# Kernel optimization log

Measured on AMD Instinct MI355X. Metric: run time of the kernel, lower is better.

Reference implementation:

```python
import jax, jax.numpy as jnp
import numpy as np

D = 512; H = 8; L = 6; DFF = 2048; V = 32000
B = 2; S_SRC = 1024; S_TRG = 1024
PAD_ID = 0
DH = D // H

def posenc(S, d):
    pos = np.arange(S)[:, None].astype(np.float32)
    i = np.arange(0, d, 2)[None, :].astype(np.float32)
    ang = pos / (10000.0 ** (i / d))
    pe = np.zeros((S, d), np.float32)
    pe[:, 0::2] = np.sin(ang)
    pe[:, 1::2] = np.cos(ang)
    return jnp.asarray(pe)

def layernorm(x, s, b):
    m = jnp.mean(x, -1, keepdims=True)
    v = jnp.var(x, -1, keepdims=True)
    return (x - m) * jax.lax.rsqrt(v + 1e-5) * s + b

def split_heads(x):
    b, s, _ = x.shape
    return x.reshape(b, s, H, DH).transpose(0, 2, 1, 3)  # [B,H,S,DH]

def merge_heads(x):
    b, h, s, dh = x.shape
    return x.transpose(0, 2, 1, 3).reshape(b, s, h * dh)

def attn(q, k, v, mask):
    # q,k,v: [B,H,Sq,DH]/[B,H,Sk,DH]; mask True = blocked, broadcastable to [B,H,Sq,Sk]
    scores = jnp.einsum('bhqd,bhkd->bhqk', q, k) * (DH ** -0.5)
    scores = jnp.where(mask, -1e9, scores)
    p = jax.nn.softmax(scores, axis=-1)
    return merge_heads(jnp.einsum('bhqk,bhkd->bhqd', p, v))

def setup_inputs() -> dict:
    key = jax.random.key(0)
    ks = iter(jax.random.split(key, 64))
    g = lambda shape, s=0.02: (jax.random.normal(next(ks), shape, jnp.float32) * s)
    inp = {}
    inp['batch_src'] = jax.random.randint(next(ks), (B, S_SRC), 0, V, jnp.int32)
    inp['trg_teacher'] = jax.random.randint(next(ks), (B, S_TRG), 0, V, jnp.int32)
    inp['src_emb'] = g((V, D)); inp['trg_emb'] = g((V, D))
    inp['fc_w'] = g((D, V)); inp['fc_b'] = jnp.zeros((V,), jnp.float32)
    # encoder layer stacks [L, ...]
    inp['enc_wqkv'] = g((L, D, 3 * D)); inp['enc_wo'] = g((L, D, D))
    inp['enc_ln1s'] = jnp.ones((L, D)); inp['enc_ln1b'] = jnp.zeros((L, D))
    inp['enc_w1'] = g((L, D, DFF)); inp['enc_b1'] = jnp.zeros((L, DFF))
    inp['enc_w2'] = g((L, DFF, D)); inp['enc_b2'] = jnp.zeros((L, D))
    inp['enc_ln2s'] = jnp.ones((L, D)); inp['enc_ln2b'] = jnp.zeros((L, D))
    # decoder layer stacks
    inp['dec_wqkv'] = g((L, D, 3 * D)); inp['dec_wo'] = g((L, D, D))
    inp['dec_ln1s'] = jnp.ones((L, D)); inp['dec_ln1b'] = jnp.zeros((L, D))
    inp['dec_wq'] = g((L, D, D)); inp['dec_wkv'] = g((L, D, 2 * D))
    inp['dec_woc'] = g((L, D, D))
    inp['dec_ln2s'] = jnp.ones((L, D)); inp['dec_ln2b'] = jnp.zeros((L, D))
    inp['dec_w1'] = g((L, D, DFF)); inp['dec_b1'] = jnp.zeros((L, DFF))
    inp['dec_w2'] = g((L, DFF, D)); inp['dec_b2'] = jnp.zeros((L, D))
    inp['dec_ln3s'] = jnp.ones((L, D)); inp['dec_ln3b'] = jnp.zeros((L, D))
    return inp

def reference(batch_src, trg_teacher, src_emb, trg_emb, fc_w, fc_b,
              enc_wqkv, enc_wo, enc_ln1s, enc_ln1b, enc_w1, enc_b1, enc_w2, enc_b2, enc_ln2s, enc_ln2b,
              dec_wqkv, dec_wo, dec_ln1s, dec_ln1b, dec_wq, dec_wkv, dec_woc, dec_ln2s, dec_ln2b,
              dec_w1, dec_b1, dec_w2, dec_b2, dec_ln3s, dec_ln3b):
    enc_mask = (batch_src == PAD_ID)[:, None, None, :]             # [B,1,1,S_src]
    causal = jnp.triu(jnp.ones((S_TRG, S_TRG), bool), 1)[None, None]  # [1,1,S,S]

    # ---- encoder ----
    x = src_emb[batch_src] * (D ** 0.5) + posenc(S_SRC, D)

    def enc_layer(x, p):
        wqkv, wo, l1s, l1b, w1, b1, w2, b2, l2s, l2b = p
        q, k, v = jnp.split(x @ wqkv, 3, axis=-1)
        o = attn(split_heads(q), split_heads(k), split_heads(v), enc_mask) @ wo
        x = layernorm(x + o, l1s, l1b)
        h = jax.nn.relu(x @ w1 + b1) @ w2 + b2
        return layernorm(x + h, l2s, l2b), None

    enc_out, _ = jax.lax.scan(enc_layer, x,
        (enc_wqkv, enc_wo, enc_ln1s, enc_ln1b, enc_w1, enc_b1, enc_w2, enc_b2, enc_ln2s, enc_ln2b))

    # ---- decoder (teacher forcing) ----
    y = trg_emb[trg_teacher] * (D ** 0.5) + posenc(S_TRG, D)

    def dec_layer(y, p):
        (wqkv, wo, l1s, l1b, wq, wkv, woc, l2s, l2b, w1, b1, w2, b2, l3s, l3b) = p
        q, k, v = jnp.split(y @ wqkv, 3, axis=-1)
        o = attn(split_heads(q), split_heads(k), split_heads(v), causal) @ wo
        y = layernorm(y + o, l1s, l1b)
        qc = y @ wq
        kc, vc = jnp.split(enc_out @ wkv, 2, axis=-1)
        oc = attn(split_heads(qc), split_heads(kc), split_heads(vc), enc_mask) @ woc
        y = layernorm(y + oc, l2s, l2b)
        h = jax.nn.relu(y @ w1 + b1) @ w2 + b2
        return layernorm(y + h, l3s, l3b), None

    dec_out, _ = jax.lax.scan(dec_layer, y,
        (dec_wqkv, dec_wo, dec_ln1s, dec_ln1b, dec_wq, dec_wkv, dec_woc, dec_ln2s, dec_ln2b,
         dec_w1, dec_b1, dec_w2, dec_b2, dec_ln3s, dec_ln3b))

    logits = dec_out @ fc_w + fc_b  # [B, S_TRG, V]
    return logits
```

## Files before the change

kernel.cpp:

```cpp
#include <hip/hip_runtime.h>
#include <cmath>

#define Dm   512
#define Hn   8
#define Ln   6
#define DFFm 2048
#define Vm   32000
#define Bn   2
#define Sn   1024
#define DHm  64
#define Mrows (Bn*Sn)

typedef unsigned short ushort_t;
typedef __attribute__((ext_vector_type(8))) short          s16x8;
typedef __attribute__((ext_vector_type(8))) unsigned short u16x8;
typedef __attribute__((ext_vector_type(4))) float          f32x4;

__device__ __forceinline__ ushort_t f2bf(float x) {
    union { float f; unsigned u; } un; un.f = x;
    unsigned r = un.u + 0x7fffu + ((un.u >> 16) & 1u);
    return (ushort_t)(r >> 16);
}

template<int TR, int NW>
__device__ __forceinline__ void stage_tile(const ushort_t* __restrict__ src, int ld,
                                           ushort_t* lds, int k0, int w, int lane)
{
    constexpr int CH = TR / (8 * NW);
    #pragma unroll
    for (int c = 0; c < CH; ++c) {
        const int rb = (w * CH + c) * 8;
        const int r  = rb + (lane >> 3);
        const ushort_t* gp = src + (size_t)r * ld + k0
                           + (((lane & 7) ^ ((lane >> 3) & 7)) << 3);
        __builtin_amdgcn_global_load_lds(
            (const __attribute__((address_space(1))) void*)gp,
            (__attribute__((address_space(3))) void*)(lds + rb * 64),
            16, 0, 0);
    }
}

__device__ __forceinline__ s16x8 ldrd(const ushort_t* lds, int r, int st)
{
    return *(const s16x8*)&lds[r * 64 + ((st ^ (r & 7)) << 3)];
}

template<int TM, int TN, int NW, bool OBF, bool BIAS, bool RELU, bool VTOUT, bool SWZ, bool RES>
__global__ __launch_bounds__(NW * 64) void gemm_bf(
    const ushort_t* __restrict__ A, const ushort_t* __restrict__ Bt,
    void* __restrict__ Cv, const float* __restrict__ bias,
    int K, int lda, int ldb, int ldc,
    long A_sb, long A_sh, long B_sb, long B_sh, long C_sb, long C_sh, int nh,
    ushort_t* __restrict__ VTp, int voff, const float* __restrict__ Xres)
{
    constexpr int WC = NW / 2;
    constexpr int FI = TM / 32;
    constexpr int FJ = TN / (16 * WC);
    __shared__ __align__(16) ushort_t As[2][TM * 64];
    __shared__ __align__(16) ushort_t Bs[2][TN * 64];

    const int z = blockIdx.z, b = z / nh, h = z - b * nh;
    A  += (size_t)b * A_sb + (size_t)h * A_sh;
    Bt += (size_t)b * B_sb + (size_t)h * B_sh;

    int bx = blockIdx.x, by = blockIdx.y;
    if constexpr (SWZ) {
        const int ncol = gridDim.x, nrow = gridDim.y;
        const int total = ncol * nrow;
        const int flat = bx + by * ncol;
        const int per = total >> 3;
        const int g = (flat & 7) * per + (flat >> 3);
        bx = g / nrow;
        by = g - bx * nrow;
    }

    const int tid  = threadIdx.x;
    const int w    = tid >> 6, lane = tid & 63;
    const int m0   = by * TM, n0 = bx * TN;
    const int rw   = (w / WC) * (TM / 2);
    const int cn   = (w % WC) * (TN / WC);
    const int l15  = lane & 15, l4 = lane >> 4;

    const ushort_t* Ab = A + (size_t)m0 * lda;
    const ushort_t* Bb = Bt + (size_t)n0 * ldb;

    f32x4 acc[FI][FJ] = {};

    stage_tile<TM, NW>(Ab, lda, As[0], 0, w, lane);
    stage_tile<TN, NW>(Bb, ldb, Bs[0], 0, w, lane);
    __syncthreads();

    const int nk = K >> 6;
    for (int t = 0; t < nk; ++t) {
        const int cur = t & 1;
        if (t + 1 < nk) {
            stage_tile<TM, NW>(Ab, lda, As[cur ^ 1], (t + 1) << 6, w, lane);
            stage_tile<TN, NW>(Bb, ldb, Bs[cur ^ 1], (t + 1) << 6, w, lane);
        }
        #pragma unroll
        for (int ks = 0; ks < 2; ++ks) {
            const int st = ks * 4 + l4;
            s16x8 av[FI], bv[FJ];
            #pragma unroll
            for (int i = 0; i < FI; ++i) av[i] = ldrd(As[cur], rw + i * 16 + l15, st);
            #pragma unroll
            for (int j = 0; j < FJ; ++j) bv[j] = ldrd(Bs[cur], cn + j * 16 + l15, st);
            #pragma unroll
            for (int i = 0; i < FI; ++i)
                #pragma unroll
                for (int j = 0; j < FJ; ++j)
                    acc[i][j] = __builtin_amdgcn_mfma_f32_16x16x32_bf16(
                                    av[i], bv[j], acc[i][j], 0, 0, 0);
        }
        __syncthreads();
    }

    const int colb = n0 + cn + l15;
    const int rowb = m0 + rw + (l4 << 2);
    float bvv[FJ];
    #pragma unroll
    for (int j = 0; j < FJ; ++j) bvv[j] = BIAS ? bias[colb + j * 16] : 0.f;

    if constexpr (OBF) {
        ushort_t* C = (ushort_t*)Cv + (size_t)b * C_sb + (size_t)h * C_sh;
        #pragma unroll
        for (int i = 0; i < FI; ++i)
            #pragma unroll
            for (int r = 0; r < 4; ++r) {
                const int row = rowb + i * 16 + r;
                #pragma unroll
                for (int j = 0; j < FJ; ++j) {
                    float v = acc[i][j][r] + bvv[j];
                    if (RELU) v = fmaxf(v, 0.f);
                    const int col = colb + j * 16;
                    if (VTOUT && col >= voff) {
                        const int hc = (col - voff) >> 6, d = (col - voff) & 63;
                        const int zz = (row >> 10) * 8 + hc;
                        VTp[(size_t)zz * (64 * Sn) + (size_t)d * Sn + (row & (Sn - 1))] = f2bf(v);
                    } else {
                        C[(size_t)row * ldc + col] = f2bf(v);
                    }
                }
            }
    } else {
        float* C = (float*)Cv + (size_t)b * C_sb + (size_t)h * C_sh;
        #pragma unroll
        for (int i = 0; i < FI; ++i)
            #pragma unroll
            for (int r = 0; r < 4; ++r) {
                const size_t row = rowb + i * 16 + r;
                #pragma unroll
                for (int j = 0; j < FJ; ++j) {
                    float v = acc[i][j][r] + bvv[j];
                    if (RES) v += Xres[row * ldc + colb + j * 16];
                    if (RELU) v = fmaxf(v, 0.f);
                    C[row * ldc + colb + j * 16] = v;
                }
            }
    }
}

template<int MODE>
__global__ __launch_bounds__(512) void flash_attn(
    const ushort_t* __restrict__ Qp, const ushort_t* __restrict__ Kp,
    const ushort_t* __restrict__ VTp, ushort_t* __restrict__ AO,
    const int* __restrict__ tok, int ldq, int ldk)
{
    __shared__ __align__(16) ushort_t Ks[2][2][64 * 64];
    __shared__ __align__(16) ushort_t Vs[2][2][64 * 64];
    __shared__ __align__(16) ushort_t Ps[8][16 * 64];
    __shared__ float msk[Sn];
    __shared__ float mrg[4][64][25];

    const int z = blockIdx.y, b = z >> 3, h = z & 7;
    const int qb = blockIdx.x * 64;
    const int tid = threadIdx.x, w = tid >> 6, lane = tid & 63;
    const int g = w >> 2, w4 = w & 3;
    const int l15 = lane & 15, l4 = lane >> 4;

    const ushort_t* Qbase = Qp + (size_t)b * Sn * ldq + h * 64;
    const ushort_t* Kbase = Kp + (size_t)b * Sn * ldk + h * 64;
    const ushort_t* Vbase = VTp + (size_t)z * 64 * Sn;
    ushort_t* Obase = AO + ((size_t)(b * Sn + qb)) * Dm + h * 64;

    if (MODE == 0) {
        const int* tb = tok + (size_t)b * Sn;
        for (int i = tid; i < Sn; i += 512) msk[i] = (tb[i] == 0) ? 1.f : 0.f;
    }

    const int qrow = qb + w4 * 16 + l15;
    s16x8 qv[2];
    qv[0] = *(const s16x8*)(Qbase + (size_t)qrow * ldq + l4 * 8);
    qv[1] = *(const s16x8*)(Qbase + (size_t)qrow * ldq + 32 + l4 * 8);

    f32x4 o[4] = {};
    float m[4], lsum[4];
    #pragma unroll
    for (int r = 0; r < 4; ++r) { m[r] = -1e30f; lsum[r] = 0.f; }

    const int nt = (MODE == 1) ? (qb / 64 + 1) : (Sn / 64);
    const int nIt = (nt + 1) >> 1;

    if (g < nt) {
        stage_tile<64, 4>(Kbase + (size_t)(g * 64) * ldk, ldk, Ks[g][0], 0, w4, lane);
        stage_tile<64, 4>(Vbase, Sn, Vs[g][0], g * 64, w4, lane);
    }
    __syncthreads();

    for (int it = 0; it < nIt; ++it) {
        const int kt = 2 * it + g;
        const int cur = it & 1;
        if (kt + 2 < nt) {
            stage_tile<64, 4>(Kbase + (size_t)((kt + 2) * 64) * ldk, ldk, Ks[g][cur ^ 1], 0, w4, lane);
            stage_tile<64, 4>(Vbase, Sn, Vs[g][cur ^ 1], (kt + 2) * 64, w4, lane);
        }
        if (kt < nt) {
            f32x4 s[4] = {};
            #pragma unroll
            for (int ks = 0; ks < 2; ++ks) {
                const int st = ks * 4 + l4;
                #pragma unroll
                for (int j = 0; j < 4; ++j) {
                    s16x8 bv = ldrd(Ks[g][cur], j * 16 + l15, st);
                    s[j] = __builtin_amdgcn_mfma_f32_16x16x32_bf16(qv[ks], bv, s[j], 0, 0, 0);
                }
            }

            #pragma unroll
            for (int j = 0; j < 4; ++j) {
                const int col = kt * 64 + j * 16 + l15;
                #pragma unroll
                for (int r = 0; r < 4; ++r) {
                    float v = s[j][r] * 0.125f;
                    if (MODE == 0) { if (msk[col] != 0.f) v = -1e9f; }
                    else           { if (col > qb + w4 * 16 + l4 * 4 + r) v = -1e9f; }
                    s[j][r] = v;
                }
            }

            float mt[4];
            #pragma unroll
            for (int r = 0; r < 4; ++r)
                mt[r] = fmaxf(fmaxf(s[0][r], s[1][r]), fmaxf(s[2][r], s[3][r]));
            #pragma unroll
            for (int mk = 1; mk < 16; mk <<= 1)
                #pragma unroll
                for (int r = 0; r < 4; ++r)
                    mt[r] = fmaxf(mt[r], __shfl_xor(mt[r], mk));

            float al[4];
            #pragma unroll
            for (int r = 0; r < 4; ++r) {
                const float mn = fmaxf(m[r], mt[r]);
                al[r] = __expf(m[r] - mn);
                m[r] = mn;
            }

            float rs[4] = {0.f, 0.f, 0.f, 0.f};
            ushort_t* pw = Ps[w];
            #pragma unroll
            for (int j = 0; j < 4; ++j) {
                const int slot = j * 2 + (l15 >> 3), e = l15 & 7;
                #pragma unroll
                for (int r = 0; r < 4; ++r) {
                    const float pvv = __expf(s[j][r] - m[r]);
                    rs[r] += pvv;
                    const int row = l4 * 4 + r;
                    pw[row * 64 + ((slot ^ (row & 7)) << 3) + e] = f2bf(pvv);
                }
            }
            #pragma unroll
            for (int mk = 1; mk < 16; mk <<= 1)
                #pragma unroll
                for (int r = 0; r < 4; ++r)
                    rs[r] += __shfl_xor(rs[r], mk);
            #pragma unroll
            for (int r = 0; r < 4; ++r) lsum[r] = lsum[r] * al[r] + rs[r];

            #pragma unroll
            for (int jd = 0; jd < 4; ++jd)
                #pragma unroll
                for (int r = 0; r < 4; ++r)
                    o[jd][r] *= al[r];
            #pragma unroll
            for (int ks2 = 0; ks2 < 2; ++ks2) {
                const int st2 = ks2 * 4 + l4;
                s16x8 pa = ldrd(pw, l15, st2);
                #pragma unroll
                for (int jd = 0; jd < 4; ++jd) {
                    s16x8 bv2 = ldrd(Vs[g][cur], jd * 16 + l15, st2);
                    o[jd] = __builtin_amdgcn_mfma_f32_16x16x32_bf16(pa, bv2, o[jd], 0, 0, 0);
                }
            }
        }
        __syncthreads();
    }

    if (g == 1) {
        float* mp = mrg[w4][lane];
        #pragma unroll
        for (int jd = 0; jd < 4; ++jd)
            #pragma unroll
            for (int r = 0; r < 4; ++r)
                mp[jd * 4 + r] = o[jd][r];
        #pragma unroll
        for (int r = 0; r < 4; ++r) { mp[16 + r] = m[r]; mp[20 + r] = lsum[r]; }
    }
    __syncthreads();
    if (g == 0) {
        const float* mp = mrg[w4][lane];
        float a0[4], a1[4], inv[4];
        #pragma unroll
        for (int r = 0; r < 4; ++r) {
            const float m1 = mp[16 + r];
            const float mm = fmaxf(m[r], m1);
            a0[r] = __expf(m[r] - mm);
            a1[r] = __expf(m1 - mm);
            inv[r] = 1.f / (lsum[r] * a0[r] + mp[20 + r] * a1[r]);
        }
        #pragma unroll
        for (int jd = 0; jd < 4; ++jd)
            #pragma unroll
            for (int r = 0; r < 4; ++r)
                Obase[(size_t)(w4 * 16 + l4 * 4 + r) * Dm + jd * 16 + l15] =
                    f2bf((o[jd][r] * a0[r] + mp[jd * 4 + r] * a1[r]) * inv[r]);
    }
}

struct WEnt { const float* src; ushort_t* dst; int R, C, tile0; };
struct WPack { WEnt e[12]; };

__global__ __launch_bounds__(256) void wcvt_all(WPack p)
{
    const int bid = blockIdx.x;
    int i = 0;
    #pragma unroll
    for (int k = 1; k < 12; ++k) if (bid >= p.e[k].tile0) i = k;
    const WEnt wd = p.e[i];
    const int rel = bid - wd.tile0;
    const int tC = wd.C >> 5, tR = wd.R >> 5;
    const int tpl = tC * tR;
    const int l = rel / tpl, t2 = rel - l * tpl;
    const int ty = t2 / tC, tx = t2 - ty * tC;

    const float* in  = wd.src + (size_t)l * wd.R * wd.C;
    ushort_t*    out = wd.dst + (size_t)l * wd.R * wd.C;

    __shared__ float tbuf[32][33];
    const int r0 = ty * 32, c0 = tx * 32;
    const int tid = threadIdx.x;
    const int r = tid >> 5, c = tid & 31;
    #pragma unroll
    for (int q = 0; q < 4; ++q)
        tbuf[r + q * 8][c] = in[(size_t)(r0 + r + q * 8) * wd.C + c0 + c];
    __syncthreads();
    const int c2 = tid >> 5, r2 = tid & 31;
    #pragma unroll
    for (int q = 0; q < 4; ++q)
        out[(size_t)(c0 + c2 + q * 8) * wd.R + r0 + r2] = f2bf(tbuf[r2][c2 + q * 8]);
}

__global__ __launch_bounds__(256) void ln_only(
    const float* __restrict__ s_in, float* __restrict__ x,
    const float* __restrict__ s, const float* __restrict__ bb,
    ushort_t* __restrict__ xbf)
{
    const long row = blockIdx.x;
    const int t = threadIdx.x;
    const float* sr = s_in + row * Dm;
    float v0 = sr[t];
    float v1 = sr[t + 256];

    float sum = v0 + v1, ssq = v0 * v0 + v1 * v1;
    __shared__ float red[8];
    for (int off = 32; off; off >>= 1) {
        sum += __shfl_down(sum, off);
        ssq += __shfl_down(ssq, off);
    }
    const int lane = t & 63, w = t >> 6;
    if (lane == 0) { red[w] = sum; red[4 + w] = ssq; }
    __syncthreads();
    sum = red[0] + red[1] + red[2] + red[3];
    ssq = red[4] + red[5] + red[6] + red[7];

    const float mean = sum * (1.f / Dm);
    const float var  = ssq * (1.f / Dm) - mean * mean;
    const float r = rsqrtf(var + 1e-5f);
    const float r0 = (v0 - mean) * r * s[t] + bb[t];
    const float r1 = (v1 - mean) * r * s[t + 256] + bb[t + 256];
    x[row * Dm + t] = r0; x[row * Dm + t + 256] = r1;
    xbf[row * Dm + t] = f2bf(r0);
    xbf[row * Dm + t + 256] = f2bf(r1);
}

__global__ __launch_bounds__(256) void embed_pe(
    const int* __restrict__ tokA, const float* __restrict__ embA,
    float* __restrict__ outA, ushort_t* __restrict__ outbfA,
    const int* __restrict__ tokB, const float* __restrict__ embB,
    float* __restrict__ outB, ushort_t* __restrict__ outbfB)
{
    const int bs = blockIdx.x;
    const int s = bs % Sn;
    const int t = threadIdx.x;
    const int*      tok   = blockIdx.y ? tokB : tokA;
    const float*    emb   = blockIdx.y ? embB : embA;
    float*          out   = blockIdx.y ? outB : outA;
    ushort_t*       outbf = blockIdx.y ? outbfB : outbfA;
    const int token = tok[bs];
    #pragma unroll
    for (int r = 0; r < 2; ++r) {
        const int d = t + r * 256;
        const int i = d & ~1;
        const float ang = (float)s * powf(10000.0f, -(float)i / (float)Dm);
        const float pe = (d & 1) ? cosf(ang) : sinf(ang);
        const float v = emb[(size_t)token * Dm + d] * 22.627416997969522f + pe;
        out[(size_t)bs * Dm + d] = v;
        outbf[(size_t)bs * Dm + d] = f2bf(v);
    }
}

extern "C" void kernel_launch(void* const* d_in, const int* in_sizes, int n_in,
                              void* d_out, int out_size, void* d_ws, size_t ws_size,
                              hipStream_t stream)
{
    const int*   batch_src = (const int*)d_in[0];
    const int*   trg       = (const int*)d_in[1];
    const float* src_emb   = (const float*)d_in[2];
    const float* trg_emb   = (const float*)d_in[3];
    const float* fc_w      = (const float*)d_in[4];
    const float* fc_b      = (const float*)d_in[5];
    const float* enc_wqkv  = (const float*)d_in[6];
    const float* enc_wo    = (const float*)d_in[7];
    const float* enc_ln1s  = (const float*)d_in[8];
    const float* enc_ln1b  = (const float*)d_in[9];
    const float* enc_w1    = (const float*)d_in[10];
    const float* enc_b1    = (const float*)d_in[11];
    const float* enc_w2    = (const float*)d_in[12];
    const float* enc_b2    = (const float*)d_in[13];
    const float* enc_ln2s  = (const float*)d_in[14];
    const float* enc_ln2b  = (const float*)d_in[15];
    const float* dec_wqkv  = (const float*)d_in[16];
    const float* dec_wo    = (const float*)d_in[17];
    const float* dec_ln1s  = (const float*)d_in[18];
    const float* dec_ln1b  = (const float*)d_in[19];
    const float* dec_wq    = (const float*)d_in[20];
    const float* dec_wkv   = (const float*)d_in[21];
    const float* dec_woc   = (const float*)d_in[22];
    const float* dec_ln2s  = (const float*)d_in[23];
    const float* dec_ln2b  = (const float*)d_in[24];
    const float* dec_w1    = (const float*)d_in[25];
    const float* dec_b1    = (const float*)d_in[26];
    const float* dec_w2    = (const float*)d_in[27];
    const float* dec_b2    = (const float*)d_in[28];
    const float* dec_ln3s  = (const float*)d_in[29];
    const float* dec_ln3b  = (const float*)d_in[30];
    (void)in_sizes; (void)n_in; (void)out_size; (void)ws_size;

    char* p = (char*)d_ws;
    auto alloc = [&](size_t bytes) { char* r = p; p += (bytes + 255) & ~(size_t)255; return r; };
    float*    X     = (float*)alloc((size_t)Mrows * Dm * 4);
    float*    Y     = (float*)alloc((size_t)Mrows * Dm * 4);
    float*    O     = (float*)alloc((size_t)Mrows * Dm * 4);
    ushort_t* Xbf   = (ushort_t*)alloc((size_t)Mrows * Dm * 2);
    ushort_t* Ybf   = (ushort_t*)alloc((size_t)Mrows * Dm * 2);
    ushort_t* QKVbf = (ushort_t*)alloc((size_t)Mrows * 3 * Dm * 2);
    ushort_t* AObf  = (ushort_t*)alloc((size_t)Mrows * Dm * 2);
    ushort_t* FHbf  = (ushort_t*)alloc((size_t)Mrows * DFFm * 2);
    ushort_t* QCbf  = (ushort_t*)alloc((size_t)Mrows * Dm * 2);
    ushort_t* KVbf  = (ushort_t*)alloc((size_t)Mrows * 2 * Dm * 2);
    ushort_t* VT    = (ushort_t*)alloc((size_t)16 * DHm * Sn * 2);
    ushort_t* ewqkv_t = (ushort_t*)alloc((size_t)Ln * 3 * Dm * Dm * 2);
    ushort_t* ewo_t   = (ushort_t*)alloc((size_t)Ln * Dm * Dm * 2);
    ushort_t* ew1_t   = (ushort_t*)alloc((size_t)Ln * DFFm * Dm * 2);
    ushort_t* ew2_t   = (ushort_t*)alloc((size_t)Ln * Dm * DFFm * 2);
    ushort_t* dwqkv_t = (ushort_t*)alloc((size_t)Ln * 3 * Dm * Dm * 2);
    ushort_t* dwo_t   = (ushort_t*)alloc((size_t)Ln * Dm * Dm * 2);
    ushort_t* dwq_t   = (ushort_t*)alloc((size_t)Ln * Dm * Dm * 2);
    ushort_t* dwkv_t  = (ushort_t*)alloc((size_t)Ln * 2 * Dm * Dm * 2);
    ushort_t* dwoc_t  = (ushort_t*)alloc((size_t)Ln * Dm * Dm * 2);
    ushort_t* dw1_t   = (ushort_t*)alloc((size_t)Ln * DFFm * Dm * 2);
    ushort_t* dw2_t   = (ushort_t*)alloc((size_t)Ln * Dm * DFFm * 2);
    ushort_t* fcw_t   = (ushort_t*)alloc((size_t)Vm * Dm * 2);

    {
        WPack pk;
        auto set = [&](int i, const float* s, ushort_t* d, int R, int C, int nl, int& acc) {
            pk.e[i] = { s, d, R, C, acc };
            acc += (R >> 5) * (C >> 5) * nl;
        };
        int acc = 0;
        set(0,  enc_wqkv, ewqkv_t, Dm,   3 * Dm, Ln, acc);
        set(1,  enc_wo,   ewo_t,   Dm,   Dm,     Ln, acc);
        set(2,  enc_w1,   ew1_t,   Dm,   DFFm,   Ln, acc);
        set(3,  enc_w2,   ew2_t,   DFFm, Dm,     Ln, acc);
        set(4,  dec_wqkv, dwqkv_t, Dm,   3 * Dm, Ln, acc);
        set(5,  dec_wo,   dwo_t,   Dm,   Dm,     Ln, acc);
        set(6,  dec_wq,   dwq_t,   Dm,   Dm,     Ln, acc);
        set(7,  dec_wkv,  dwkv_t,  Dm,   2 * Dm, Ln, acc);
        set(8,  dec_woc,  dwoc_t,  Dm,   Dm,     Ln, acc);
        set(9,  dec_w1,   dw1_t,   Dm,   DFFm,   Ln, acc);
        set(10, dec_w2,   dw2_t,   DFFm, Dm,     Ln, acc);
        set(11, fc_w,     fcw_t,   Dm,   Vm,     1,  acc);
        wcvt_all<<<acc, 256, 0, stream>>>(pk);
    }

    embed_pe<<<dim3(Mrows, 2), 256, 0, stream>>>(
        batch_src, src_emb, X, Xbf, trg, trg_emb, Y, Ybf);

    for (int l = 0; l < Ln; ++l) {
        gemm_bf<64,128,8,true,false,false,true,false,false><<<dim3(12, 32, 1), 512, 0, stream>>>(
            Xbf, ewqkv_t + (size_t)l * 3 * Dm * Dm, QKVbf, nullptr,
            Dm, Dm, Dm, 3 * Dm, 0,0,0,0,0,0, 1, VT, 2 * Dm, nullptr);
        flash_attn<0><<<dim3(16, 16), 512, 0, stream>>>(
            QKVbf, QKVbf + Dm, VT, AObf, batch_src, 3 * Dm, 3 * Dm);
        gemm_bf<64,64,8,false,false,false,false,false,true><<<dim3(8, 32, 1), 512, 0, stream>>>(
            AObf, ewo_t + (size_t)l * Dm * Dm, O, nullptr,
            Dm, Dm, Dm, Dm, 0,0,0,0,0,0, 1, nullptr, 0, X);
        ln_only<<<Mrows, 256, 0, stream>>>(O, X, enc_ln1s + l * Dm, enc_ln1b + l * Dm, Xbf);
        gemm_bf<64,128,8,true,true,true,false,false,false><<<dim3(16, 32, 1), 512, 0, stream>>>(
            Xbf, ew1_t + (size_t)l * DFFm * Dm, FHbf, enc_b1 + l * DFFm,
            Dm, Dm, Dm, DFFm, 0,0,0,0,0,0, 1, nullptr, 0, nullptr);
        gemm_bf<64,64,8,false,true,false,false,false,true><<<dim3(8, 32, 1), 512, 0, stream>>>(
            FHbf, ew2_t + (size_t)l * Dm * DFFm, O, enc_b2 + l * Dm,
            DFFm, DFFm, DFFm, Dm, 0,0,0,0,0,0, 1, nullptr, 0, X);
        ln_only<<<Mrows, 256, 0, stream>>>(O, X, enc_ln2s + l * Dm, enc_ln2b + l * Dm, Xbf);
    }

    for (int l = 0; l < Ln; ++l) {
        gemm_bf<64,128,8,true,false,false,true,false,false><<<dim3(12, 32, 1), 512, 0, stream>>>(
            Ybf, dwqkv_t + (size_t)l * 3 * Dm * Dm, QKVbf, nullptr,
            Dm, Dm, Dm, 3 * Dm, 0,0,0,0,0,0, 1, VT, 2 * Dm, nullptr);
        flash_attn<1><<<dim3(16, 16), 512, 0, stream>>>(
            QKVbf, QKVbf + Dm, VT, AObf, nullptr, 3 * Dm, 3 * Dm);
        gemm_bf<64,64,8,false,false,false,false,false,true><<<dim3(8, 32, 1), 512, 0, stream>>>(
            AObf, dwo_t + (size_t)l * Dm * Dm, O, nullptr,
            Dm, Dm, Dm, Dm, 0,0,0,0,0,0, 1, nullptr, 0, Y);
        ln_only<<<Mrows, 256, 0, stream>>>(O, Y, dec_ln1s + l * Dm, dec_ln1b + l * Dm, Ybf);

        gemm_bf<64,64,8,true,false,false,false,false,false><<<dim3(8, 32, 1), 512, 0, stream>>>(
            Ybf, dwq_t + (size_t)l * Dm * Dm, QCbf, nullptr,
            Dm, Dm, Dm, Dm, 0,0,0,0,0,0, 1, nullptr, 0, nullptr);
        gemm_bf<64,128,8,true,false,false,true,false,false><<<dim3(8, 32, 1), 512, 0, stream>>>(
            Xbf, dwkv_t + (size_t)l * 2 * Dm * Dm, KVbf, nullptr,
            Dm, Dm, Dm, 2 * Dm, 0,0,0,0,0,0, 1, VT, Dm, nullptr);
        flash_attn<0><<<dim3(16, 16), 512, 0, stream>>>(
            QCbf, KVbf, VT, AObf, batch_src, Dm, 2 * Dm);
        gemm_bf<64,64,8,false,false,false,false,false,true><<<dim3(8, 32, 1), 512, 0, stream>>>(
            AObf, dwoc_t + (size_t)l * Dm * Dm, O, nullptr,
            Dm, Dm, Dm, Dm, 0,0,0,0,0,0, 1, nullptr, 0, Y);
        ln_only<<<Mrows, 256, 0, stream>>>(O, Y, dec_ln2s + l * Dm, dec_ln2b + l * Dm, Ybf);

        gemm_bf<64,128,8,true,true,true,false,false,false><<<dim3(16, 32, 1), 512, 0, stream>>>(
            Ybf, dw1_t + (size_t)l * DFFm * Dm, FHbf, dec_b1 + l * DFFm,
            Dm, Dm, Dm, DFFm, 0,0,0,0,0,0, 1, nullptr, 0, nullptr);
        gemm_bf<64,64,8,false,true,false,false,false,true><<<dim3(8, 32, 1), 512, 0, stream>>>(
            FHbf, dw2_t + (size_t)l * Dm * DFFm, O, dec_b2 + l * Dm,
            DFFm, DFFm, DFFm, Dm, 0,0,0,0,0,0, 1, nullptr, 0, Y);
        ln_only<<<Mrows, 256, 0, stream>>>(O, Y, dec_ln3s + l * Dm, dec_ln3b + l * Dm, Ybf);
    }

    gemm_bf<128,128,8,false,true,false,false,true,false><<<dim3(Vm / 128, 16, 1), 512, 0, stream>>>(
        Ybf, fcw_t, (float*)d_out, fc_b,
        Dm, Dm, Dm, Vm, 0,0,0,0,0,0, 1, nullptr, 0, nullptr);
}
```

Before: 1.593 ms.

## Batch cross-attention KV projections for all layers and fuse decoder Q projections

Cross-attention K/V projections of the encoder output run once for all six decoder layers in a single batched GEMM (grid z = layers), writing into per-layer KV and V-transpose caches. The decoder's self-attention QKV weights and cross-attention Q weights are packed into one 4*D-wide matrix, so one GEMM replaces two per layer. Several GEMM instantiations also drop from 8 to 4 waves per block. This cuts launches and gives larger grids, at the cost of extra workspace and changed per-thread tiling.

```diff
diff --git a/kernel.cpp b/kernel.cpp
--- a/kernel.cpp
+++ b/kernel.cpp
@@ -51,7 +51,7 @@
     void* __restrict__ Cv, const float* __restrict__ bias,
     int K, int lda, int ldb, int ldc,
     long A_sb, long A_sh, long B_sb, long B_sh, long C_sb, long C_sh, int nh,
-    ushort_t* __restrict__ VTp, int voff, const float* __restrict__ Xres)
+    ushort_t* __restrict__ VTp, int voff, long VT_sz, const float* __restrict__ Xres)
 {
     constexpr int WC = NW / 2;
     constexpr int FI = TM / 32;
@@ -62,6 +62,7 @@
     const int z = blockIdx.z, b = z / nh, h = z - b * nh;
     A  += (size_t)b * A_sb + (size_t)h * A_sh;
     Bt += (size_t)b * B_sb + (size_t)h * B_sh;
+    ushort_t* VTl = VTp + (size_t)z * VT_sz;
 
     int bx = blockIdx.x, by = blockIdx.y;
     if constexpr (SWZ) {
@@ -133,10 +134,10 @@
                     float v = acc[i][j][r] + bvv[j];
                     if (RELU) v = fmaxf(v, 0.f);
                     const int col = colb + j * 16;
-                    if (VTOUT && col >= voff) {
+                    if (VTOUT && col >= voff && col < voff + 512) {
                         const int hc = (col - voff) >> 6, d = (col - voff) & 63;
                         const int zz = (row >> 10) * 8 + hc;
-                        VTp[(size_t)zz * (64 * Sn) + (size_t)d * Sn + (row & (Sn - 1))] = f2bf(v);
+                        VTl[(size_t)zz * (64 * Sn) + (size_t)d * Sn + (row & (Sn - 1))] = f2bf(v);
                     } else {
                         C[(size_t)row * ldc + col] = f2bf(v);
                     }
@@ -327,7 +328,7 @@
     }
 }
 
-struct WEnt { const float* src; ushort_t* dst; int R, C, tile0; };
+struct WEnt { const float* src; ushort_t* dst; int R, C, tile0; long dls; };
 struct WPack { WEnt e[12]; };
 
 __global__ __launch_bounds__(256) void wcvt_all(WPack p)
@@ -344,7 +345,7 @@
     const int ty = t2 / tC, tx = t2 - ty * tC;
 
     const float* in  = wd.src + (size_t)l * wd.R * wd.C;
-    ushort_t*    out = wd.dst + (size_t)l * wd.R * wd.C;
+    ushort_t*    out = wd.dst + (size_t)l * wd.dls;
 
     __shared__ float tbuf[32][33];
     const int r0 = ty * 32, c0 = tx * 32;
@@ -464,18 +465,18 @@
     ushort_t* Xbf   = (ushort_t*)alloc((size_t)Mrows * Dm * 2);
     ushort_t* Ybf   = (ushort_t*)alloc((size_t)Mrows * Dm * 2);
     ushort_t* QKVbf = (ushort_t*)alloc((size_t)Mrows * 3 * Dm * 2);
+    ushort_t* QKVQ  = (ushort_t*)alloc((size_t)Mrows * 4 * Dm * 2);
     ushort_t* AObf  = (ushort_t*)alloc((size_t)Mrows * Dm * 2);
     ushort_t* FHbf  = (ushort_t*)alloc((size_t)Mrows * DFFm * 2);
-    ushort_t* QCbf  = (ushort_t*)alloc((size_t)Mrows * Dm * 2);
-    ushort_t* KVbf  = (ushort_t*)alloc((size_t)Mrows * 2 * Dm * 2);
     ushort_t* VT    = (ushort_t*)alloc((size_t)16 * DHm * Sn * 2);
+    ushort_t* KVC   = (ushort_t*)alloc((size_t)Ln * Mrows * 2 * Dm * 2);
+    ushort_t* VTC   = (ushort_t*)alloc((size_t)Ln * 16 * DHm * Sn * 2);
     ushort_t* ewqkv_t = (ushort_t*)alloc((size_t)Ln * 3 * Dm * Dm * 2);
     ushort_t* ewo_t   = (ushort_t*)alloc((size_t)Ln * Dm * Dm * 2);
     ushort_t* ew1_t   = (ushort_t*)alloc((size_t)Ln * DFFm * Dm * 2);
     ushort_t* ew2_t   = (ushort_t*)alloc((size_t)Ln * Dm * DFFm * 2);
-    ushort_t* dwqkv_t = (ushort_t*)alloc((size_t)Ln * 3 * Dm * Dm * 2);
+    ushort_t* dwqkvq_t= (ushort_t*)alloc((size_t)Ln * 4 * Dm * Dm * 2);
     ushort_t* dwo_t   = (ushort_t*)alloc((size_t)Ln * Dm * Dm * 2);
-    ushort_t* dwq_t   = (ushort_t*)alloc((size_t)Ln * Dm * Dm * 2);
     ushort_t* dwkv_t  = (ushort_t*)alloc((size_t)Ln * 2 * Dm * Dm * 2);
     ushort_t* dwoc_t  = (ushort_t*)alloc((size_t)Ln * Dm * Dm * 2);
     ushort_t* dw1_t   = (ushort_t*)alloc((size_t)Ln * DFFm * Dm * 2);
@@ -484,82 +485,87 @@
 
     {
         WPack pk;
-        auto set = [&](int i, const float* s, ushort_t* d, int R, int C, int nl, int& acc) {
-            pk.e[i] = { s, d, R, C, acc };
+        auto set = [&](int i, const float* s, ushort_t* d, int R, int C, int nl,
+                       long dls, int& acc) {
+            pk.e[i] = { s, d, R, C, acc, dls };
             acc += (R >> 5) * (C >> 5) * nl;
         };
         int acc = 0;
-        set(0,  enc_wqkv, ewqkv_t, Dm,   3 * Dm, Ln, acc);
-        set(1,  enc_wo,   ewo_t,   Dm,   Dm,     Ln, acc);
-        set(2,  enc_w1,   ew1_t,   Dm,   DFFm,   Ln, acc);
-        set(3,  enc_w2,   ew2_t,   DFFm, Dm,     Ln, acc);
-        set(4,  dec_wqkv, dwqkv_t, Dm,   3 * Dm, Ln, acc);
-        set(5,  dec_wo,   dwo_t,   Dm,   Dm,     Ln, acc);
-        set(6,  dec_wq,   dwq_t,   Dm,   Dm,     Ln, acc);
-        set(7,  dec_wkv,  dwkv_t,  Dm,   2 * Dm, Ln, acc);
-        set(8,  dec_woc,  dwoc_t,  Dm,   Dm,     Ln, acc);
-        set(9,  dec_w1,   dw1_t,   Dm,   DFFm,   Ln, acc);
-        set(10, dec_w2,   dw2_t,   DFFm, Dm,     Ln, acc);
-        set(11, fc_w,     fcw_t,   Dm,   Vm,     1,  acc);
+        const long L4 = (long)4 * Dm * Dm;
+        set(0,  enc_wqkv, ewqkv_t, Dm,   3 * Dm, Ln, (long)3 * Dm * Dm, acc);
+        set(1,  enc_wo,   ewo_t,   Dm,   Dm,     Ln, (long)Dm * Dm,     acc);
+        set(2,  enc_w1,   ew1_t,   Dm,   DFFm,   Ln, (long)Dm * DFFm,   acc);
+        set(3,  enc_w2,   ew2_t,   DFFm, Dm,     Ln, (long)Dm * DFFm,   acc);
+        set(4,  dec_wqkv, dwqkvq_t,                Dm, 3 * Dm, Ln, L4,  acc);
+        set(5,  dec_wq,   dwqkvq_t + (size_t)3 * Dm * Dm, Dm, Dm, Ln, L4, acc);
+        set(6,  dec_wo,   dwo_t,   Dm,   Dm,     Ln, (long)Dm * Dm,     acc);
+        set(7,  dec_wkv,  dwkv_t,  Dm,   2 * Dm, Ln, (long)2 * Dm * Dm, acc);
+        set(8,  dec_woc,  dwoc_t,  Dm,   Dm,     Ln, (long)Dm * Dm,     acc);
+        set(9,  dec_w1,   dw1_t,   Dm,   DFFm,   Ln, (long)Dm * DFFm,   acc);
+        set(10, dec_w2,   dw2_t,   DFFm, Dm,     Ln, (long)Dm * DFFm,   acc);
+        set(11, fc_w,     fcw_t,   Dm,   Vm,     1,  (long)Dm * Vm,     acc);
         wcvt_all<<<acc, 256, 0, stream>>>(pk);
     }
 
     embed_pe<<<dim3(Mrows, 2), 256, 0, stream>>>(
         batch_src, src_emb, X, Xbf, trg, trg_emb, Y, Ybf);
 
+    const long VTs = (long)16 * DHm * Sn;
+
     for (int l = 0; l < Ln; ++l) {
-        gemm_bf<64,128,8,true,false,false,true,false,false><<<dim3(12, 32, 1), 512, 0, stream>>>(
+        gemm_bf<64,128,4,true,false,false,true,false,false><<<dim3(12, 32, 1), 256, 0, stream>>>(
             Xbf, ewqkv_t + (size_t)l * 3 * Dm * Dm, QKVbf, nullptr,
-            Dm, Dm, Dm, 3 * Dm, 0,0,0,0,0,0, 1, VT, 2 * Dm, nullptr);
+            Dm, Dm, Dm, 3 * Dm, 0,0,0,0,0,0, 1, VT, 2 * Dm, 0, nullptr);
         flash_attn<0><<<dim3(16, 16), 512, 0, stream>>>(
             QKVbf, QKVbf + Dm, VT, AObf, batch_src, 3 * Dm, 3 * Dm);
         gemm_bf<64,64,8,false,false,false,false,false,true><<<dim3(8, 32, 1), 512, 0, stream>>>(
             AObf, ewo_t + (size_t)l * Dm * Dm, O, nullptr,
-            Dm, Dm, Dm, Dm, 0,0,0,0,0,0, 1, nullptr, 0, X);
+            Dm, Dm, Dm, Dm, 0,0,0,0,0,0, 1, nullptr, 0, 0, X);
         ln_only<<<Mrows, 256, 0, stream>>>(O, X, enc_ln1s + l * Dm, enc_ln1b + l * Dm, Xbf);
-        gemm_bf<64,128,8,true,true,true,false,false,false><<<dim3(16, 32, 1), 512, 0, stream>>>(
+        gemm_bf<64,128,4,true,true,true,false,false,false><<<dim3(16, 32, 1), 256, 0, stream>>>(
             Xbf, ew1_t + (size_t)l * DFFm * Dm, FHbf, enc_b1 + l * DFFm,
-            Dm, Dm, Dm, DFFm, 0,0,0,0,0,0, 1, nullptr, 0, nullptr);
+            Dm, Dm, Dm, DFFm, 0,0,0,0,0,0, 1, nullptr, 0, 0, nullptr);
         gemm_bf<64,64,8,false,true,false,false,false,true><<<dim3(8, 32, 1), 512, 0, stream>>>(
             FHbf, ew2_t + (size_t)l * Dm * DFFm, O, enc_b2 + l * Dm,
-            DFFm, DFFm, DFFm, Dm, 0,0,0,0,0,0, 1, nullptr, 0, X);
+            DFFm, DFFm, DFFm, Dm, 0,0,0,0,0,0, 1, nullptr, 0, 0, X);
         ln_only<<<Mrows, 256, 0, stream>>>(O, X, enc_ln2s + l * Dm, enc_ln2b + l * Dm, Xbf);
     }
 
+    gemm_bf<64,128,4,true,false,false,true,false,false><<<dim3(8, 32, Ln), 256, 0, stream>>>(
+        Xbf, dwkv_t, KVC, nullptr,
+        Dm, Dm, Dm, 2 * Dm,
+        0, 0, (long)2 * Dm * Dm, 0, (long)Mrows * 2 * Dm, 0, 1,
+        VTC, Dm, VTs, nullptr);
+
     for (int l = 0; l < Ln; ++l) {
-        gemm_bf<64,128,8,true,false,false,true,false,false><<<dim3(12, 32, 1), 512, 0, stream>>>(
-            Ybf, dwqkv_t + (size_t)l * 3 * Dm * Dm, QKVbf, nullptr,
-            Dm, Dm, Dm, 3 * Dm, 0,0,0,0,0,0, 1, VT, 2 * Dm, nullptr);
+        gemm_bf<64,128,4,true,false,false,true,false,false><<<dim3(16, 32, 1), 256, 0, stream>>>(
+            Ybf, dwqkvq_t + (size_t)l * 4 * Dm * Dm, QKVQ, nullptr,
+            Dm, Dm, Dm, 4 * Dm, 0,0,0,0,0,0, 1, VT, 2 * Dm, 0, nullptr);
         flash_attn<1><<<dim3(16, 16), 512, 0, stream>>>(
-            QKVbf, QKVbf + Dm, VT, AObf, nullptr, 3 * Dm, 3 * Dm);
+            QKVQ, QKVQ + Dm, VT, AObf, nullptr, 4 * Dm, 4 * Dm);
         gemm_bf<64,64,8,false,false,false,false,false,true><<<dim3(8, 32, 1), 512, 0, stream>>>(
             AObf, dwo_t + (size_t)l * Dm * Dm, O, nullptr,
-            Dm, Dm, Dm, Dm, 0,0,0,0,0,0, 1, nullptr, 0, Y);
+            Dm, Dm, Dm, Dm, 0,0,0,0,0,0, 1, nullptr, 0, 0, Y);
         ln_only<<<Mrows, 256, 0, stream>>>(O, Y, dec_ln1s + l * Dm, dec_ln1b + l * Dm, Ybf);
 
-        gemm_bf<64,64,8,true,false,false,false,false,false><<<dim3(8, 32, 1), 512, 0, stream>>>(
-            Ybf, dwq_t + (size_t)l * Dm * Dm, QCbf, nullptr,
-            Dm, Dm, Dm, Dm, 0,0,0,0,0,0, 1, nullptr, 0, nullptr);
-        gemm_bf<64,128,8,true,false,false,true,false,false><<<dim3(8, 32, 1), 512, 0, stream>>>(
-            Xbf, dwkv_t + (size_t)l * 2 * Dm * Dm, KVbf, nullptr,
-            Dm, Dm, Dm, 2 * Dm, 0,0,0,0,0,0, 1, VT, Dm, nullptr);
         flash_attn<0><<<dim3(16, 16), 512, 0, stream>>>(
-            QCbf, KVbf, VT, AObf, batch_src, Dm, 2 * Dm);
+            QKVQ + 3 * Dm, KVC + (size_t)l * Mrows * 2 * Dm,
+            VTC + (size_t)l * VTs, AObf, batch_src, 4 * Dm, 2 * Dm);
         gemm_bf<64,64,8,false,false,false,false,false,true><<<dim3(8, 32, 1), 512, 0, stream>>>(
             AObf, dwoc_t + (size_t)l * Dm * Dm, O, nullptr,
-            Dm, Dm, Dm, Dm, 0,0,0,0,0,0, 1, nullptr, 0, Y);
+            Dm, Dm, Dm, Dm, 0,0,0,0,0,0, 1, nullptr, 0, 0, Y);
         ln_only<<<Mrows, 256, 0, stream>>>(O, Y, dec_ln2s + l * Dm, dec_ln2b + l * Dm, Ybf);
 
-        gemm_bf<64,128,8,true,true,true,false,false,false><<<dim3(16, 32, 1), 512, 0, stream>>>(
+        gemm_bf<64,128,4,true,true,true,false,false,false><<<dim3(16, 32, 1), 256, 0, stream>>>(
             Ybf, dw1_t + (size_t)l * DFFm * Dm, FHbf, dec_b1 + l * DFFm,
-            Dm, Dm, Dm, DFFm, 0,0,0,0,0,0, 1, nullptr, 0, nullptr);
+            Dm, Dm, Dm, DFFm, 0,0,0,0,0,0, 1, nullptr, 0, 0, nullptr);
         gemm_bf<64,64,8,false,true,false,false,false,true><<<dim3(8, 32, 1), 512, 0, stream>>>(
             FHbf, dw2_t + (size_t)l * Dm * DFFm, O, dec_b2 + l * Dm,
-            DFFm, DFFm, DFFm, Dm, 0,0,0,0,0,0, 1, nullptr, 0, Y);
+            DFFm, DFFm, DFFm, Dm, 0,0,0,0,0,0, 1, nullptr, 0, 0, Y);
         ln_only<<<Mrows, 256, 0, stream>>>(O, Y, dec_ln3s + l * Dm, dec_ln3b + l * Dm, Ybf);
     }
 
-    gemm_bf<128,128,8,false,true,false,false,true,false><<<dim3(Vm / 128, 16, 1), 512, 0, stream>>>(
+    gemm_bf<128,128,4,false,true,false,false,true,false><<<dim3(Vm / 128, 16, 1), 256, 0, stream>>>(
         Ybf, fcw_t, (float*)d_out, fc_b,
-        Dm, Dm, Dm, Vm, 0,0,0,0,0,0, 1, nullptr, 0, nullptr);
-}
+        Dm, Dm, Dm, Vm, 0,0,0,0,0,0, 1, nullptr, 0, 0, nullptr);
+}
```

Result: no change. 1.587 ms (-0.4%).
